# Kernel optimization log

Measured on AMD Instinct MI355X. Metric: run time of the kernel, lower is better.

## Reference

```python
import jax, jax.numpy as jnp
import numpy as np

NUM_EMBS = 1024
EMB_DIM = 128
Z_SHAPE = (16, 4096, EMB_DIM)


def setup_inputs() -> dict:
    key = jax.random.key(0)
    k_z, k_c = jax.random.split(key)
    z = jax.random.normal(k_z, Z_SHAPE, dtype=jnp.float32)
    # torch init: uniform(-1/num_embs, 1/num_embs)
    codebook = jax.random.uniform(
        k_c, (NUM_EMBS, EMB_DIM), dtype=jnp.float32,
        minval=-1.0 / NUM_EMBS, maxval=1.0 / NUM_EMBS)
    return {"z": z, "codebook": codebook}


def reference(z, codebook):
    """Vector quantization forward (nbooks=1, balance=False).

    Returns (z_q with straight-through estimator, quant_loss, commit_loss, indices).
    """
    K, D = codebook.shape
    zf = z.reshape(-1, D)  # [M, D]
    dist = (
        jnp.sum(zf * zf, axis=1, keepdims=True)
        - 2.0 * (zf @ codebook.T)
        + jnp.sum(codebook * codebook, axis=1)[None, :]
    )
    idx = jnp.argmin(dist, axis=1)  # [M]
    # one-hot @ codebook == gather (same math, efficient form)
    z_q = codebook[idx].reshape(z.shape)
    quant_loss = jnp.mean((jax.lax.stop_gradient(z_q) - z) ** 2, axis=-1)
    commit_loss = jnp.mean((z_q - jax.lax.stop_gradient(z)) ** 2, axis=-1)
    # straight-through estimator
    z_q_ste = z + jax.lax.stop_gradient(z_q - z)
    indices = idx.reshape(z.shape[:-1])
    return z_q_ste, quant_loss, commit_loss, indices
```

## Files before the change

kernel.cpp:

```cpp
#include <hip/hip_runtime.h>
#include <hip/hip_bf16.h>

namespace {
constexpr int D       = 128;
constexpr int K       = 1024;
constexpr int M_TOTAL = 65536;
constexpr int BM      = 128;
constexpr int NCT     = K / 16;
constexpr float TAU   = 5.0e-5f;
constexpr size_t WS_CN   = 0;
constexpr size_t WS_BH   = 4096;
constexpr size_t WS_BL   = 4096 + 262144;
constexpr size_t WS_REQ  = 4096 + 2 * 262144;
constexpr size_t WS_CBT  = WS_REQ;
constexpr size_t WS_REQ2 = WS_REQ + 524288;
}

typedef short bf16x8 __attribute__((ext_vector_type(8)));
typedef float f32x4  __attribute__((ext_vector_type(4)));

static __device__ __forceinline__ unsigned short bfbits(float x) {
  __hip_bfloat16 h = __float2bfloat16(x);
  return *reinterpret_cast<unsigned short*>(&h);
}
static __device__ __forceinline__ float bfhi2f(unsigned short h) {
  return __uint_as_float(((unsigned)h) << 16);
}
static __device__ __forceinline__ void split8(float4 a, float4 b,
                                              bf16x8& ph, bf16x8& pl) {
  float v[8] = {a.x, a.y, a.z, a.w, b.x, b.y, b.z, b.w};
#pragma unroll
  for (int e = 0; e < 8; ++e) {
    unsigned short h = bfbits(v[e]);
    unsigned short l = bfbits(v[e] - bfhi2f(h));
    ph[e] = (short)h;
    pl[e] = (short)l;
  }
}
static __device__ __forceinline__ float np_norm128(const float* p) {
  float r8[8];
#pragma unroll
  for (int j = 0; j < 8; ++j) r8[j] = __fmul_rn(p[j], p[j]);
  for (int i = 8; i < D; i += 8) {
#pragma unroll
    for (int j = 0; j < 8; ++j)
      r8[j] = __fadd_rn(r8[j], __fmul_rn(p[i + j], p[i + j]));
  }
  return __fadd_rn(__fadd_rn(__fadd_rn(r8[0], r8[1]), __fadd_rn(r8[2], r8[3])),
                   __fadd_rn(__fadd_rn(r8[4], r8[5]), __fadd_rn(r8[6], r8[7])));
}

__global__ void vq_prep_all(const float* __restrict__ cb, float* __restrict__ Cn,
                            int* __restrict__ cnt,
                            short* __restrict__ Bh, short* __restrict__ Bl,
                            float4* __restrict__ cbT4) {
  const int b = blockIdx.x, t = threadIdx.x;
  if (b < 4) {
    int k = b * 256 + t;
    if (b == 0 && t == 0) *cnt = 0;
    if (k < K) Cn[k] = np_norm128(cb + (size_t)k * D);
  } else if (b < 68) {
    int g = (b - 4) * 256 + t;
    int code = (g >> 8) * 16 + (g & 15);
    int d0   = ((g >> 6) & 3) * 32 + ((g >> 4) & 3) * 8;
    const float* p = cb + (size_t)code * D + d0;
    float4 a = *reinterpret_cast<const float4*>(p);
    float4 bb = *reinterpret_cast<const float4*>(p + 4);
    bf16x8 ph, pl;
    split8(a, bb, ph, pl);
    *reinterpret_cast<bf16x8*>(Bh + (size_t)g * 8) = ph;
    *reinterpret_cast<bf16x8*>(Bl + (size_t)g * 8) = pl;
  } else {
    int g = (b - 68) * 256 + t;
    int d = g >> 8, tt = g & 255;
    float4 v;
    v.x = cb[(size_t)(4 * tt + 0) * D + d];
    v.y = cb[(size_t)(4 * tt + 1) * D + d];
    v.z = cb[(size_t)(4 * tt + 2) * D + d];
    v.w = cb[(size_t)(4 * tt + 3) * D + d];
    cbT4[g] = v;
  }
}

__global__ __launch_bounds__(256, 2) void vq_score(
    const float* __restrict__ z, const float* __restrict__ cb,
    const float* __restrict__ Cn,
    const short* __restrict__ BhG, const short* __restrict__ BlG,
    float* __restrict__ out_zq, float* __restrict__ out_q,
    float* __restrict__ out_iF, int* __restrict__ cnt, int* __restrict__ list) {
  __shared__ __align__(16) short Bbuf[4][8][512];
  __shared__ float CnS[K];
  __shared__ int   idxW[4][32];

  const int t    = threadIdx.x;
  const int wave = t >> 6;
  const int lane = t & 63;
  const int col  = lane & 15;
  const int baseRow = blockIdx.x * BM;

  for (int i = t; i < K; i += 256) CnS[i] = Cn[i];

  bf16x8 ah[2][4], al[2][4];
#pragma unroll
  for (int set = 0; set < 2; ++set) {
    const float* zL = z + (size_t)(baseRow + wave * 32 + set * 16 + col) * D + (lane >> 4) * 8;
#pragma unroll
    for (int ks = 0; ks < 4; ++ks) {
      float4 a = *reinterpret_cast<const float4*>(zL + ks * 32);
      float4 b = *reinterpret_cast<const float4*>(zL + ks * 32 + 4);
      split8(a, b, ah[set][ks], al[set][ks]);
    }
  }

  float s1[2][4], s2[2][4]; int i1[2][4];
#pragma unroll
  for (int s = 0; s < 2; ++s)
#pragma unroll
    for (int i = 0; i < 4; ++i) {
      s1[s][i] = 3.402823466e+38f; s2[s][i] = 3.402823466e+38f; i1[s][i] = 0;
    }

#define STAGE(ct_, bi_)                                                             \
  { _Pragma("unroll")                                                               \
    for (int i_ = 0; i_ < 2; ++i_) {                                                \
      int c_  = wave * 2 + i_;                                                      \
      int p_  = c_ >> 2, ks_ = c_ & 3;                                              \
      const short* gsrc_ = (p_ ? BlG : BhG) +                                       \
                           (size_t)(((ct_) * 4 + ks_) * 64 + lane) * 8;             \
      __builtin_amdgcn_global_load_lds(                                             \
          (const __attribute__((address_space(1))) void*)gsrc_,                     \
          (__attribute__((address_space(3))) void*)&Bbuf[bi_][c_][0], 16, 0, 0);    \
    } }

#define COMP(bi_, ct_)                                                              \
  { bf16x8 bh_c[4], bl_c[4];                                                        \
    _Pragma("unroll")                                                               \
    for (int ks_ = 0; ks_ < 4; ++ks_) {                                             \
      bh_c[ks_] = *reinterpret_cast<const bf16x8*>(&Bbuf[bi_][ks_][lane * 8]);      \
      bl_c[ks_] = *reinterpret_cast<const bf16x8*>(&Bbuf[bi_][4 + ks_][lane * 8]);  \
    }                                                                               \
    const int code_ = (ct_) * 16 + col;                                             \
    const float cn_ = CnS[code_];                                                   \
    __builtin_amdgcn_s_setprio(1);                                                  \
    _Pragma("unroll")                                                               \
    for (int set_ = 0; set_ < 2; ++set_) {                                          \
      f32x4 aA = (f32x4){0.f,0.f,0.f,0.f};                                          \
      f32x4 aB = (f32x4){0.f,0.f,0.f,0.f};                                          \
      f32x4 aC = (f32x4){0.f,0.f,0.f,0.f};                                          \
      _Pragma("unroll")                                                             \
      for (int ks_ = 0; ks_ < 4; ++ks_) {                                           \
        aA = __builtin_amdgcn_mfma_f32_16x16x32_bf16(ah[set_][ks_], bh_c[ks_], aA, 0,0,0); \
        aB = __builtin_amdgcn_mfma_f32_16x16x32_bf16(ah[set_][ks_], bl_c[ks_], aB, 0,0,0); \
        aC = __builtin_amdgcn_mfma_f32_16x16x32_bf16(al[set_][ks_], bh_c[ks_], aC, 0,0,0); \
      }                                                                             \
      _Pragma("unroll")                                                             \
      for (int reg_ = 0; reg_ < 4; ++reg_) {                                        \
        float S = fmaf(-2.0f, (aA[reg_] + aB[reg_]) + aC[reg_], cn_);               \
        if (S < s1[set_][reg_]) { s2[set_][reg_] = s1[set_][reg_];                  \
                                  s1[set_][reg_] = S; i1[set_][reg_] = code_; }     \
        else if (S < s2[set_][reg_]) { s2[set_][reg_] = S; }                        \
      }                                                                             \
    }                                                                               \
    __builtin_amdgcn_s_setprio(0); }

#define PHASE(t_, bi_)                                                              \
  { asm volatile("s_waitcnt vmcnt(4)" ::: "memory");                                \
    __builtin_amdgcn_s_barrier();                                                   \
    __builtin_amdgcn_sched_barrier(0);                                              \
    COMP(bi_, t_);                                                                  \
    STAGE(((t_) + 3) & 63, ((bi_) + 3) & 3); }

  __syncthreads();
  STAGE(0, 0); STAGE(1, 1); STAGE(2, 2);
  for (int g = 0; g < NCT; g += 4) {
    PHASE(g + 0, 0);
    PHASE(g + 1, 1);
    PHASE(g + 2, 2);
    PHASE(g + 3, 3);
  }
#undef PHASE
#undef STAGE
#undef COMP

#pragma unroll
  for (int m = 1; m < 16; m <<= 1) {
#pragma unroll
    for (int set = 0; set < 2; ++set)
#pragma unroll
      for (int reg = 0; reg < 4; ++reg) {
        float os1 = __shfl_xor(s1[set][reg], m, 64);
        float os2 = __shfl_xor(s2[set][reg], m, 64);
        int   oi  = __shfl_xor(i1[set][reg], m, 64);
        if (os1 < s1[set][reg]) {
          s2[set][reg] = fminf(s1[set][reg], os2);
          s1[set][reg] = os1; i1[set][reg] = oi;
        } else {
          s2[set][reg] = fminf(s2[set][reg], os1);
        }
      }
  }

  if (col == 0) {
#pragma unroll
    for (int set = 0; set < 2; ++set)
#pragma unroll
      for (int reg = 0; reg < 4; ++reg) {
        int wr = set * 16 + (lane >> 4) * 4 + reg;
        idxW[wave][wr] = i1[set][reg];
        if (s2[set][reg] - s1[set][reg] < TAU) {
          int p = atomicAdd(cnt, 1);
          if (p < M_TOTAL - 1) list[p] = (int)(baseRow + wave * 32 + wr);
        }
      }
  }

  {
    const int r = lane >> 1, q = lane & 1;
    const size_t m = (size_t)baseRow + wave * 32 + r;
    const int idx = idxW[wave][r];
    const float4* cq = reinterpret_cast<const float4*>(cb + (size_t)idx * D) + q * 16;
    const float4* zr = reinterpret_cast<const float4*>(z + m * D) + q * 16;
    float4*       o4 = reinterpret_cast<float4*>(out_zq + m * D) + q * 16;
    float sum = 0.f;
#pragma unroll
    for (int e = 0; e < 16; ++e) {
      float4 cv = cq[e];
      float4 zv = zr[e];
      float dx = cv.x - zv.x, dy = cv.y - zv.y, dz = cv.z - zv.z, dw = cv.w - zv.w;
      float4 st;
      st.x = zv.x + dx; st.y = zv.y + dy; st.z = zv.z + dz; st.w = zv.w + dw;
      o4[e] = st;
      sum = fmaf(dx, dx, sum); sum = fmaf(dy, dy, sum);
      sum = fmaf(dz, dz, sum); sum = fmaf(dw, dw, sum);
    }
    sum += __shfl_xor(sum, 1, 64);
    if (q == 0) {
      float lv = sum * 0.0078125f;
      out_q[m]  = lv;
      out_iF[m] = (float)idx;
    }
  }
}

__global__ __launch_bounds__(256, 4) void vq_rescan_cbT(
    const float* __restrict__ z, const float* __restrict__ cb,
    const float4* __restrict__ cbT4, const float* __restrict__ Cn,
    const int* __restrict__ cnt, const int* __restrict__ list,
    float* __restrict__ out_zq, float* __restrict__ out_q,
    float* __restrict__ out_iF) {
  __shared__ __align__(16) float Zs[D];
  __shared__ float sRed[256];
  __shared__ int   iRed[256];
  const int t = threadIdx.x;
  int n = *cnt; if (n > M_TOTAL - 1) n = M_TOTAL - 1;

  for (int it = blockIdx.x; it < n; it += gridDim.x) {
    const int row = list[it];
    if (t < 32) {
      reinterpret_cast<float4*>(Zs)[t] =
          reinterpret_cast<const float4*>(z + (size_t)row * D)[t];
    }
    __syncthreads();

    float a0 = 0.f, a1 = 0.f, a2 = 0.f, a3 = 0.f;
#pragma unroll 8
    for (int d = 0; d < D; ++d) {
      float  zv = Zs[d];
      float4 cv = cbT4[(d << 8) + t];
      a0 = fmaf(zv, cv.x, a0);
      a1 = fmaf(zv, cv.y, a1);
      a2 = fmaf(zv, cv.z, a2);
      a3 = fmaf(zv, cv.w, a3);
    }
    const float A = np_norm128(Zs);

    const int kb = t * 4;
    float bd = 3.402823466e+38f; int bi = 0;
    {
      float d0 = __fadd_rn(__fsub_rn(A, __fmul_rn(2.0f, a0)), Cn[kb + 0]);
      float d1 = __fadd_rn(__fsub_rn(A, __fmul_rn(2.0f, a1)), Cn[kb + 1]);
      float d2 = __fadd_rn(__fsub_rn(A, __fmul_rn(2.0f, a2)), Cn[kb + 2]);
      float d3 = __fadd_rn(__fsub_rn(A, __fmul_rn(2.0f, a3)), Cn[kb + 3]);
      if (d0 < bd) { bd = d0; bi = kb + 0; }
      if (d1 < bd) { bd = d1; bi = kb + 1; }
      if (d2 < bd) { bd = d2; bi = kb + 2; }
      if (d3 < bd) { bd = d3; bi = kb + 3; }
    }
    sRed[t] = bd; iRed[t] = bi;
    __syncthreads();
    for (int w = 128; w > 0; w >>= 1) {
      if (t < w) {
        float o = sRed[t + w]; int oi = iRed[t + w];
        if (o < sRed[t] || (o == sRed[t] && oi < iRed[t])) { sRed[t] = o; iRed[t] = oi; }
      }
      __syncthreads();
    }
    const int win = iRed[0];
    if (t < 32) {
      float4 zv = reinterpret_cast<const float4*>(Zs)[t];
      float4 cv = reinterpret_cast<const float4*>(cb + (size_t)win * D)[t];
      float dx = cv.x - zv.x, dy = cv.y - zv.y, dz = cv.z - zv.z, dw = cv.w - zv.w;
      float4 st;
      st.x = zv.x + dx; st.y = zv.y + dy; st.z = zv.z + dz; st.w = zv.w + dw;
      reinterpret_cast<float4*>(out_zq + (size_t)row * D)[t] = st;
      float sq = fmaf(dx, dx, fmaf(dy, dy, fmaf(dz, dz, dw * dw)));
      sq += __shfl_xor(sq, 1, 64);  sq += __shfl_xor(sq, 2, 64);
      sq += __shfl_xor(sq, 4, 64);  sq += __shfl_xor(sq, 8, 64);
      sq += __shfl_xor(sq, 16, 64);
      if (t == 0) {
        out_q[row]  = sq * 0.0078125f;
        out_iF[row] = (float)win;
      }
    }
    __syncthreads();
  }
}

__global__ void vq_copy(const float* __restrict__ q, float* __restrict__ c) {
  int m = blockIdx.x * 256 + threadIdx.x;
  c[m] = q[m];
}

__global__ __launch_bounds__(256) void vq_main_fp32(
    const float* __restrict__ z, const float* __restrict__ cb,
    const float* __restrict__ Cn,
    float* __restrict__ out_zq, float* __restrict__ out_q,
    float* __restrict__ out_c, float* __restrict__ out_i) {
  __shared__ float Zt[64 * D];
  __shared__ float Ct[64 * D];
  __shared__ float Arow[64];
  __shared__ int   idxArr[64];

  const int t  = threadIdx.x;
  const int ty = t >> 4;
  const int tx = t & 15;
  const int baseRow = blockIdx.x * 64;

  for (int s = t; s < 64 * (D / 4); s += 256) {
    int r = s >> 5, d4 = s & 31;
    float4 v = reinterpret_cast<const float4*>(z)[(size_t)(baseRow + r) * (D / 4) + d4];
    int colx = d4 ^ (r & 7);
    *reinterpret_cast<float4*>(&Zt[r * D + colx * 4]) = v;
  }
  __syncthreads();

  if (t < 64) {
    const int rs = t & 7;
    float r8[8];
#pragma unroll
    for (int j = 0; j < 8; ++j) {
      float v = Zt[t * D + (((j >> 2) ^ rs) << 2) + (j & 3)];
      r8[j] = __fmul_rn(v, v);
    }
    for (int i = 8; i < D; i += 8) {
#pragma unroll
      for (int j = 0; j < 8; ++j) {
        int d = i + j;
        float v = Zt[t * D + (((d >> 2) ^ rs) << 2) + (d & 3)];
        r8[j] = __fadd_rn(r8[j], __fmul_rn(v, v));
      }
    }
    Arow[t] = __fadd_rn(__fadd_rn(__fadd_rn(r8[0], r8[1]), __fadd_rn(r8[2], r8[3])),
                        __fadd_rn(__fadd_rn(r8[4], r8[5]), __fadd_rn(r8[6], r8[7])));
  }

  float s1[4]; int i1[4];
#pragma unroll
  for (int i = 0; i < 4; ++i) { s1[i] = 3.402823466e+38f; i1[i] = 0; }

  const int zsw = ty & 7;
  const int csw = tx & 7;

  for (int kt = 0; kt < 16; ++kt) {
    __syncthreads();
    for (int s = t; s < 64 * (D / 4); s += 256) {
      int r = s >> 5, d4 = s & 31;
      float4 v = reinterpret_cast<const float4*>(cb)[(size_t)(kt * 64 + r) * (D / 4) + d4];
      int colx = d4 ^ (r & 7);
      *reinterpret_cast<float4*>(&Ct[r * D + colx * 4]) = v;
    }
    __syncthreads();

    float acc[4][4];
#pragma unroll
    for (int i = 0; i < 4; ++i)
#pragma unroll
      for (int j = 0; j < 4; ++j) acc[i][j] = 0.f;

    for (int d4 = 0; d4 < 32; ++d4) {
      float4 za[4], cv[4];
      int zc = (d4 ^ zsw) * 4;
      int cc = (d4 ^ csw) * 4;
#pragma unroll
      for (int i = 0; i < 4; ++i)
        za[i] = *reinterpret_cast<const float4*>(&Zt[(ty + 16 * i) * D + zc]);
#pragma unroll
      for (int j = 0; j < 4; ++j)
        cv[j] = *reinterpret_cast<const float4*>(&Ct[(tx + 16 * j) * D + cc]);
#pragma unroll
      for (int i = 0; i < 4; ++i)
#pragma unroll
        for (int j = 0; j < 4; ++j) {
          acc[i][j] = fmaf(za[i].x, cv[j].x, acc[i][j]);
          acc[i][j] = fmaf(za[i].y, cv[j].y, acc[i][j]);
          acc[i][j] = fmaf(za[i].z, cv[j].z, acc[i][j]);
          acc[i][j] = fmaf(za[i].w, cv[j].w, acc[i][j]);
        }
    }

    float ch[4]; int kg[4];
#pragma unroll
    for (int j = 0; j < 4; ++j) {
      kg[j] = kt * 64 + tx + 16 * j;
      ch[j] = Cn[kg[j]];
    }
#pragma unroll
    for (int i = 0; i < 4; ++i) {
      float a = Arow[ty + 16 * i];
#pragma unroll
      for (int j = 0; j < 4; ++j) {
        float dist = __fadd_rn(__fsub_rn(a, __fmul_rn(2.0f, acc[i][j])), ch[j]);
        if (dist < s1[i]) { s1[i] = dist; i1[i] = kg[j]; }
      }
    }
  }

#pragma unroll
  for (int m = 1; m < 16; m <<= 1) {
#pragma unroll
    for (int i = 0; i < 4; ++i) {
      float os = __shfl_xor(s1[i], m, 64);
      int   oi = __shfl_xor(i1[i], m, 64);
      if (os < s1[i] || (os == s1[i] && oi < i1[i])) { s1[i] = os; i1[i] = oi; }
    }
  }

  if (tx == 0) {
#pragma unroll
    for (int i = 0; i < 4; ++i) idxArr[ty + 16 * i] = i1[i];
  }
  __syncthreads();

  {
    int r = t >> 2, q = t & 3;
    int idx = idxArr[r];
    size_t m = (size_t)baseRow + r;
    const float4* cq = reinterpret_cast<const float4*>(cb + (size_t)idx * D);
    const float4* zr = reinterpret_cast<const float4*>(z + m * D);
    float4*       o4 = reinterpret_cast<float4*>(out_zq + m * D);
    float sum = 0.f;
#pragma unroll
    for (int e = 0; e < 8; ++e) {
      int d4 = q * 8 + e;
      float4 cv = cq[d4];
      float4 zv = zr[d4];
      float dx = cv.x - zv.x, dy = cv.y - zv.y, dz = cv.z - zv.z, dw = cv.w - zv.w;
      float4 st;
      st.x = zv.x + dx; st.y = zv.y + dy; st.z = zv.z + dz; st.w = zv.w + dw;
      o4[d4] = st;
      sum = fmaf(dx, dx, sum); sum = fmaf(dy, dy, sum);
      sum = fmaf(dz, dz, sum); sum = fmaf(dw, dw, sum);
    }
    sum += __shfl_xor(sum, 1, 64);
    sum += __shfl_xor(sum, 2, 64);
    if (q == 0) {
      float lv = sum * 0.0078125f;
      out_q[m] = lv;
      out_c[m] = lv;
      out_i[m] = (float)idx;
    }
  }
}

extern "C" void kernel_launch(void* const* d_in, const int* in_sizes, int n_in,
                              void* d_out, int out_size, void* d_ws, size_t ws_size,
                              hipStream_t stream) {
  const float* z  = (const float*)d_in[0];
  const float* cb = (const float*)d_in[1];

  float* out0 = (float*)d_out;
  float* out1 = out0 + (size_t)M_TOTAL * D;
  float* out2 = out1 + M_TOTAL;
  float* out3 = out2 + M_TOTAL;

  float* Cn = (float*)((char*)d_ws + WS_CN);
  int* cnt  = (int*)out2;
  int* list = (int*)out2 + 1;

  if (ws_size >= WS_REQ2) {
    short*  Bh   = (short*)((char*)d_ws + WS_BH);
    short*  Bl   = (short*)((char*)d_ws + WS_BL);
    float4* cbT4 = (float4*)((char*)d_ws + WS_CBT);
    vq_prep_all<<<196, 256, 0, stream>>>(cb, Cn, cnt, Bh, Bl, cbT4);
    vq_score<<<M_TOTAL / BM, 256, 0, stream>>>(z, cb, Cn, Bh, Bl,
                                               out0, out1, out3, cnt, list);
    vq_rescan_cbT<<<1024, 256, 0, stream>>>(z, cb, cbT4, Cn, cnt, list,
                                            out0, out1, out3);
    vq_copy<<<M_TOTAL / 256, 256, 0, stream>>>(out1, out2);
  } else {
    vq_prep_all<<<4, 256, 0, stream>>>(cb, Cn, cnt, nullptr, nullptr, nullptr);
    vq_main_fp32<<<M_TOTAL / 64, 256, 0, stream>>>(z, cb, Cn, out0, out1, out2, out3);
  }
}
```

Measured before the change: 114.9 us.

## Halve rows per block in VQ scoring kernel and coalesce epilogue writes

Each wave now handles 16 rows instead of 32, so the block tile shrinks to 64 rows and register use drops enough to raise the launch-bounds occupancy target from 2 to 4 blocks per CU. The gather-and-write epilogue is restructured so 32 lanes cover one row with contiguous float4 accesses and reduce the squared error with shuffles. Each block now streams the full codebook while reusing it for only half as many rows, which doubles the codebook traffic through LDS and L2.

Measured after the change: 103.9 us. -9.6%, faster.

```diff
diff --git a/kernel.cpp b/kernel.cpp
--- a/kernel.cpp
+++ b/kernel.cpp
@@ -5,7 +5,7 @@
 constexpr int D       = 128;
 constexpr int K       = 1024;
 constexpr int M_TOTAL = 65536;
-constexpr int BM      = 128;
+constexpr int BM      = 64;
 constexpr int NCT     = K / 16;
 constexpr float TAU   = 5.0e-5f;
 constexpr size_t WS_CN   = 0;
@@ -82,7 +82,7 @@
   }
 }
 
-__global__ __launch_bounds__(256, 2) void vq_score(
+__global__ __launch_bounds__(256, 4) void vq_score(
     const float* __restrict__ z, const float* __restrict__ cb,
     const float* __restrict__ Cn,
     const short* __restrict__ BhG, const short* __restrict__ BlG,
@@ -90,7 +90,7 @@
     float* __restrict__ out_iF, int* __restrict__ cnt, int* __restrict__ list) {
   __shared__ __align__(16) short Bbuf[4][8][512];
   __shared__ float CnS[K];
-  __shared__ int   idxW[4][32];
+  __shared__ int   idxW[4][16];
 
   const int t    = threadIdx.x;
   const int wave = t >> 6;
@@ -100,25 +100,22 @@
 
   for (int i = t; i < K; i += 256) CnS[i] = Cn[i];
 
-  bf16x8 ah[2][4], al[2][4];
-#pragma unroll
-  for (int set = 0; set < 2; ++set) {
-    const float* zL = z + (size_t)(baseRow + wave * 32 + set * 16 + col) * D + (lane >> 4) * 8;
+  bf16x8 ah[4], al[4];
+  {
+    const float* zL = z + (size_t)(baseRow + wave * 16 + col) * D + (lane >> 4) * 8;
 #pragma unroll
     for (int ks = 0; ks < 4; ++ks) {
       float4 a = *reinterpret_cast<const float4*>(zL + ks * 32);
       float4 b = *reinterpret_cast<const float4*>(zL + ks * 32 + 4);
-      split8(a, b, ah[set][ks], al[set][ks]);
-    }
-  }
-
-  float s1[2][4], s2[2][4]; int i1[2][4];
-#pragma unroll
-  for (int s = 0; s < 2; ++s)
-#pragma unroll
-    for (int i = 0; i < 4; ++i) {
-      s1[s][i] = 3.402823466e+38f; s2[s][i] = 3.402823466e+38f; i1[s][i] = 0;
-    }
+      split8(a, b, ah[ks], al[ks]);
+    }
+  }
+
+  float s1[4], s2[4]; int i1[4];
+#pragma unroll
+  for (int i = 0; i < 4; ++i) {
+    s1[i] = 3.402823466e+38f; s2[i] = 3.402823466e+38f; i1[i] = 0;
+  }
 
 #define STAGE(ct_, bi_)                                                             \
   { _Pragma("unroll")                                                               \
@@ -142,24 +139,20 @@
     const int code_ = (ct_) * 16 + col;                                             \
     const float cn_ = CnS[code_];                                                   \
     __builtin_amdgcn_s_setprio(1);                                                  \
+    f32x4 aA = (f32x4){0.f,0.f,0.f,0.f};                                            \
+    f32x4 aB = (f32x4){0.f,0.f,0.f,0.f};                                            \
+    f32x4 aC = (f32x4){0.f,0.f,0.f,0.f};                                            \
     _Pragma("unroll")                                                               \
-    for (int set_ = 0; set_ < 2; ++set_) {                                          \
-      f32x4 aA = (f32x4){0.f,0.f,0.f,0.f};                                          \
-      f32x4 aB = (f32x4){0.f,0.f,0.f,0.f};                                          \
-      f32x4 aC = (f32x4){0.f,0.f,0.f,0.f};                                          \
-      _Pragma("unroll")                                                             \
-      for (int ks_ = 0; ks_ < 4; ++ks_) {                                           \
-        aA = __builtin_amdgcn_mfma_f32_16x16x32_bf16(ah[set_][ks_], bh_c[ks_], aA, 0,0,0); \
-        aB = __builtin_amdgcn_mfma_f32_16x16x32_bf16(ah[set_][ks_], bl_c[ks_], aB, 0,0,0); \
-        aC = __builtin_amdgcn_mfma_f32_16x16x32_bf16(al[set_][ks_], bh_c[ks_], aC, 0,0,0); \
-      }                                                                             \
-      _Pragma("unroll")                                                             \
-      for (int reg_ = 0; reg_ < 4; ++reg_) {                                        \
-        float S = fmaf(-2.0f, (aA[reg_] + aB[reg_]) + aC[reg_], cn_);               \
-        if (S < s1[set_][reg_]) { s2[set_][reg_] = s1[set_][reg_];                  \
-                                  s1[set_][reg_] = S; i1[set_][reg_] = code_; }     \
-        else if (S < s2[set_][reg_]) { s2[set_][reg_] = S; }                        \
-      }                                                                             \
+    for (int ks_ = 0; ks_ < 4; ++ks_) {                                             \
+      aA = __builtin_amdgcn_mfma_f32_16x16x32_bf16(ah[ks_], bh_c[ks_], aA, 0,0,0);  \
+      aB = __builtin_amdgcn_mfma_f32_16x16x32_bf16(ah[ks_], bl_c[ks_], aB, 0,0,0);  \
+      aC = __builtin_amdgcn_mfma_f32_16x16x32_bf16(al[ks_], bh_c[ks_], aC, 0,0,0);  \
+    }                                                                               \
+    _Pragma("unroll")                                                               \
+    for (int reg_ = 0; reg_ < 4; ++reg_) {                                          \
+      float S = fmaf(-2.0f, (aA[reg_] + aB[reg_]) + aC[reg_], cn_);                 \
+      if (S < s1[reg_]) { s2[reg_] = s1[reg_]; s1[reg_] = S; i1[reg_] = code_; }    \
+      else if (S < s2[reg_]) { s2[reg_] = S; }                                      \
     }                                                                               \
     __builtin_amdgcn_s_setprio(0); }
 
@@ -185,59 +178,55 @@
 #pragma unroll
   for (int m = 1; m < 16; m <<= 1) {
 #pragma unroll
-    for (int set = 0; set < 2; ++set)
-#pragma unroll
-      for (int reg = 0; reg < 4; ++reg) {
-        float os1 = __shfl_xor(s1[set][reg], m, 64);
-        float os2 = __shfl_xor(s2[set][reg], m, 64);
-        int   oi  = __shfl_xor(i1[set][reg], m, 64);
-        if (os1 < s1[set][reg]) {
-          s2[set][reg] = fminf(s1[set][reg], os2);
-          s1[set][reg] = os1; i1[set][reg] = oi;
-        } else {
-          s2[set][reg] = fminf(s2[set][reg], os1);
-        }
-      }
+    for (int reg = 0; reg < 4; ++reg) {
+      float os1 = __shfl_xor(s1[reg], m, 64);
+      float os2 = __shfl_xor(s2[reg], m, 64);
+      int   oi  = __shfl_xor(i1[reg], m, 64);
+      if (os1 < s1[reg]) {
+        s2[reg] = fminf(s1[reg], os2);
+        s1[reg] = os1; i1[reg] = oi;
+      } else {
+        s2[reg] = fminf(s2[reg], os1);
+      }
+    }
   }
 
   if (col == 0) {
 #pragma unroll
-    for (int set = 0; set < 2; ++set)
-#pragma unroll
-      for (int reg = 0; reg < 4; ++reg) {
-        int wr = set * 16 + (lane >> 4) * 4 + reg;
-        idxW[wave][wr] = i1[set][reg];
-        if (s2[set][reg] - s1[set][reg] < TAU) {
-          int p = atomicAdd(cnt, 1);
-          if (p < M_TOTAL - 1) list[p] = (int)(baseRow + wave * 32 + wr);
-        }
-      }
+    for (int reg = 0; reg < 4; ++reg) {
+      int wr = (lane >> 4) * 4 + reg;
+      idxW[wave][wr] = i1[reg];
+      if (s2[reg] - s1[reg] < TAU) {
+        int p = atomicAdd(cnt, 1);
+        if (p < M_TOTAL - 1) list[p] = (int)(baseRow + wave * 16 + wr);
+      }
+    }
   }
 
   {
-    const int r = lane >> 1, q = lane & 1;
-    const size_t m = (size_t)baseRow + wave * 32 + r;
-    const int idx = idxW[wave][r];
-    const float4* cq = reinterpret_cast<const float4*>(cb + (size_t)idx * D) + q * 16;
-    const float4* zr = reinterpret_cast<const float4*>(z + m * D) + q * 16;
-    float4*       o4 = reinterpret_cast<float4*>(out_zq + m * D) + q * 16;
-    float sum = 0.f;
-#pragma unroll
-    for (int e = 0; e < 16; ++e) {
-      float4 cv = cq[e];
-      float4 zv = zr[e];
+    const float* zW  = z      + ((size_t)baseRow + wave * 16) * D;
+    float*       oW  = out_zq + ((size_t)baseRow + wave * 16) * D;
+#pragma unroll
+    for (int it = 0; it < 8; ++it) {
+      const int flat = lane + 64 * it;
+      const int r    = flat >> 5;
+      const int d4   = flat & 31;
+      const int idx  = idxW[wave][r];
+      float4 cv = reinterpret_cast<const float4*>(cb + (size_t)idx * D)[d4];
+      float4 zv = reinterpret_cast<const float4*>(zW)[flat];
       float dx = cv.x - zv.x, dy = cv.y - zv.y, dz = cv.z - zv.z, dw = cv.w - zv.w;
       float4 st;
       st.x = zv.x + dx; st.y = zv.y + dy; st.z = zv.z + dz; st.w = zv.w + dw;
-      o4[e] = st;
-      sum = fmaf(dx, dx, sum); sum = fmaf(dy, dy, sum);
-      sum = fmaf(dz, dz, sum); sum = fmaf(dw, dw, sum);
-    }
-    sum += __shfl_xor(sum, 1, 64);
-    if (q == 0) {
-      float lv = sum * 0.0078125f;
-      out_q[m]  = lv;
-      out_iF[m] = (float)idx;
+      reinterpret_cast<float4*>(oW)[flat] = st;
+      float sq = fmaf(dx, dx, fmaf(dy, dy, fmaf(dz, dz, dw * dw)));
+      sq += __shfl_xor(sq, 1, 64);  sq += __shfl_xor(sq, 2, 64);
+      sq += __shfl_xor(sq, 4, 64);  sq += __shfl_xor(sq, 8, 64);
+      sq += __shfl_xor(sq, 16, 64);
+      if ((lane & 31) == 0) {
+        size_t m = (size_t)baseRow + wave * 16 + r;
+        out_q[m]  = sq * 0.0078125f;
+        out_iF[m] = (float)idx;
+      }
     }
   }
 }
```
